# Performance work log

Measured on AMD Instinct MI355X. Metric: run time of the kernel, lower is better.

## Reference

```python
import jax, jax.numpy as jnp
import numpy as np

IN_DIMS = (8, 8, 8, 8)
OUT_DIMS = (8, 8, 8, 8)
RANK = 8
IN_FEATURES = 4096
OUT_FEATURES = 4096
BATCH = 4096


def setup_inputs() -> dict:
    key = jax.random.key(0)
    ks = jax.random.split(key, 6)
    scale = 1.0 / (IN_FEATURES ** 0.5)
    d = len(IN_DIMS)
    ranks = (1,) + (RANK,) * (d - 1) + (1,)
    cores = {}
    for k in range(d):
        shape = (ranks[k], IN_DIMS[k], OUT_DIMS[k], ranks[k + 1])
        # roughly balanced per-core scale so the dense-equivalent weight has ~1/sqrt(N) scale
        c_scale = scale ** (1.0 / d)
        cores[f"core_{k}"] = (jax.random.normal(ks[k + 1], shape, dtype=jnp.float32) * c_scale)
    x = jax.random.normal(ks[0], (BATCH, IN_FEATURES), dtype=jnp.float32)
    bias = jnp.zeros((OUT_FEATURES,), dtype=jnp.float32)
    return {"x": x, **cores, "bias": bias}


def _tt_contract(x, cores):
    # x: (B, N) with N = prod(IN_DIMS). Cores: core_k (r_{k-1}, i_k, o_k, r_k).
    # y[b, o1..od] = sum_{i,r} prod_k core_k[r_{k-1}, i_k, o_k, r_k] * x[b, i1..id]
    B = x.shape[0]
    d = len(IN_DIMS)
    # z: (Bo, r, i_k, suffix) where Bo = B * prod(out dims already contracted)
    z = x.reshape(B, 1, IN_DIMS[0], -1)
    for k, core in enumerate(cores):
        # contract current input mode and left rank against the core
        z = jnp.einsum("bris,riok->boks", z, core)  # (Bo, o_k, r_k, suffix)
        if k + 1 < d:
            Bo, ok, rk, s = z.shape
            z = z.reshape(Bo * ok, rk, IN_DIMS[k + 1], s // IN_DIMS[k + 1])
    return z.reshape(B, -1)  # (B, prod(OUT_DIMS))


def reference(x, core_0, core_1, core_2, core_3, bias):
    in_dtype = x.dtype
    xc = x.astype(core_0.dtype)
    y = _tt_contract(xc, (core_0, core_1, core_2, core_3))
    y = y + bias
    return y.astype(in_dtype)
```

## Files before the change

kernel.cpp:

```cpp
#include <hip/hip_runtime.h>
#include <hip/hip_bf16.h>


typedef __attribute__((ext_vector_type(8))) short bf16x8;
typedef __attribute__((ext_vector_type(4))) float f32x4;

#define MFMA16(a, b, c) __builtin_amdgcn_mfma_f32_16x16x32_bf16(a, b, c, 0, 0, 0)

__device__ __forceinline__ short f2bf(float f) {
    union { float f; unsigned u; } v{f};
    unsigned r = v.u + 0x7fff + ((v.u >> 16) & 1);
    return (short)(r >> 16);
}

__global__ void tt_prep(const float* __restrict__ c0, const float* __restrict__ c1,
                        const float* __restrict__ c2, const float* __restrict__ c3,
                        short* __restrict__ wpack) {
    int e    = blockIdx.x * 256 + threadIdx.x;
    int isV  = e >> 15;
    int idx  = e & 32767;
    int r2   = idx >> 12;
    int rem  = idx & 4095;
    int frag = rem >> 9;
    int lane = (rem >> 3) & 63;
    int j    = rem & 7;
    int nt = frag >> 1, kt = frag & 1;
    int k = kt * 32 + (lane >> 4) * 8 + j;
    int n = nt * 16 + (lane & 15);
    float acc = 0.f;
    if (!isV) {
        int i0 = k >> 3, i1 = k & 7, o0 = n >> 3, o1 = n & 7;
        #pragma unroll
        for (int r1 = 0; r1 < 8; ++r1)
            acc += c0[(i0 * 8 + o0) * 8 + r1] * c1[((r1 * 8 + i1) * 8 + o1) * 8 + r2];
    } else {
        int i2 = k >> 3, i3 = k & 7, o2 = n >> 3, o3 = n & 7;
        #pragma unroll
        for (int r3 = 0; r3 < 8; ++r3)
            acc += c2[((r2 * 8 + i2) * 8 + o2) * 8 + r3] * c3[(r3 * 8 + i3) * 8 + o3];
    }
    wpack[e] = f2bf(acc);
}

__global__ __launch_bounds__(512, 2)
void tt_main(const float* __restrict__ x, const float* __restrict__ bias,
             const short* __restrict__ wpack, float* __restrict__ out) {
    __shared__ short tbuf[8 * 4096];
    const int tid  = threadIdx.x;
    const int wave = tid >> 6;
    const int lane = tid & 63;
    const int lo   = lane & 15;
    const int q    = lane >> 4;
    const int b    = blockIdx.x * 8 + wave;

    short* T = &tbuf[wave * 4096];

    bf16x8 xa[4][2];
    const float* xb = x + (size_t)b * 4096;
    #pragma unroll
    for (int mt = 0; mt < 4; ++mt)
        #pragma unroll
        for (int kt = 0; kt < 2; ++kt)
            #pragma unroll
            for (int j = 0; j < 8; ++j) {
                int i01 = kt * 32 + q * 8 + j;
                int i23 = mt * 16 + lo;
                xa[mt][kt][j] = f2bf(xb[i01 * 64 + i23]);
            }

    f32x4 yacc[4][4];
    #pragma unroll
    for (int m = 0; m < 4; ++m)
        #pragma unroll
        for (int n = 0; n < 4; ++n)
            yacc[m][n] = f32x4{0.f, 0.f, 0.f, 0.f};

    const bf16x8* Up = (const bf16x8*)wpack;
    const bf16x8* Vp = (const bf16x8*)(wpack + 32768);

    for (int r2 = 0; r2 < 8; ++r2) {
        bf16x8 uf[4][2];
        #pragma unroll
        for (int nt = 0; nt < 4; ++nt)
            #pragma unroll
            for (int kt = 0; kt < 2; ++kt)
                uf[nt][kt] = Up[(r2 * 8 + nt * 2 + kt) * 64 + lane];

        #pragma unroll
        for (int mt = 0; mt < 4; ++mt) {
            f32x4 tacc[4];
            #pragma unroll
            for (int nt = 0; nt < 4; ++nt) tacc[nt] = f32x4{0.f, 0.f, 0.f, 0.f};
            #pragma unroll
            for (int kt = 0; kt < 2; ++kt)
                #pragma unroll
                for (int nt = 0; nt < 4; ++nt)
                    tacc[nt] = MFMA16(xa[mt][kt], uf[nt][kt], tacc[nt]);
            #pragma unroll
            for (int nt = 0; nt < 4; ++nt) {
                int o01 = nt * 16 + lo;
                int i23 = mt * 16 + q * 4;
                unsigned w0 = (unsigned)(unsigned short)f2bf(tacc[nt][0]) |
                              ((unsigned)(unsigned short)f2bf(tacc[nt][1]) << 16);
                unsigned w1 = (unsigned)(unsigned short)f2bf(tacc[nt][2]) |
                              ((unsigned)(unsigned short)f2bf(tacc[nt][3]) << 16);
                int byteoff = (o01 * 128 + i23 * 2) ^ ((o01 & 7) << 4);
                *(uint2*)((char*)T + byteoff) = make_uint2(w0, w1);
            }
        }

        bf16x8 vf[4][2];
        #pragma unroll
        for (int nt = 0; nt < 4; ++nt)
            #pragma unroll
            for (int kt = 0; kt < 2; ++kt)
                vf[nt][kt] = Vp[(r2 * 8 + nt * 2 + kt) * 64 + lane];

        #pragma unroll
        for (int kt = 0; kt < 2; ++kt) {
            bf16x8 ta[4];
            #pragma unroll
            for (int mt = 0; mt < 4; ++mt) {
                int o01 = mt * 16 + lo;
                int i23 = kt * 32 + q * 8;
                int byteoff = (o01 * 128 + i23 * 2) ^ ((o01 & 7) << 4);
                ta[mt] = *(const bf16x8*)((const char*)T + byteoff);
            }
            #pragma unroll
            for (int mt = 0; mt < 4; ++mt)
                #pragma unroll
                for (int nt = 0; nt < 4; ++nt)
                    yacc[mt][nt] = MFMA16(ta[mt], vf[nt][kt], yacc[mt][nt]);
        }
    }

    float* ob = out + (size_t)b * 4096;
    #pragma unroll
    for (int mt = 0; mt < 4; ++mt)
        #pragma unroll
        for (int nt = 0; nt < 4; ++nt)
            #pragma unroll
            for (int r = 0; r < 4; ++r) {
                int o01 = mt * 16 + q * 4 + r;
                int o23 = nt * 16 + lo;
                int no  = o01 * 64 + o23;
                ob[no] = yacc[mt][nt][r] + bias[no];
            }
}

extern "C" void kernel_launch(void* const* d_in, const int* in_sizes, int n_in,
                              void* d_out, int out_size, void* d_ws, size_t ws_size,
                              hipStream_t stream) {
    const float* x    = (const float*)d_in[0];
    const float* c0   = (const float*)d_in[1];
    const float* c1   = (const float*)d_in[2];
    const float* c2   = (const float*)d_in[3];
    const float* c3   = (const float*)d_in[4];
    const float* bias = (const float*)d_in[5];
    short* wpack = (short*)d_ws;

    tt_prep<<<256, 256, 0, stream>>>(c0, c1, c2, c3, wpack);
    tt_main<<<512, 512, 0, stream>>>(x, bias, wpack, (float*)d_out);
}
```

Measured before the change: 150.8 us.

## Switch to 32x32 MFMA and pass intermediate through registers via permlane swap

Reorders the two-stage contraction so the i23 modes are contracted first with 32x32x16 bf16 MFMA, and the intermediate is repacked in registers using permlane32_swap instead of being staged through LDS. The x load becomes vectorized float4 reads, and blocks shrink to 4 waves with twice as many blocks. This removes the LDS round trip and its synchronization-free but bandwidth-bound shared traffic, at the cost of more register pressure from 32x32 accumulators.

Measured after the change: 145.7 us. 1.04x faster.

```diff
diff --git a/kernel.cpp b/kernel.cpp
--- a/kernel.cpp
+++ b/kernel.cpp
@@ -3,148 +3,151 @@
 
 
 typedef __attribute__((ext_vector_type(8))) short bf16x8;
-typedef __attribute__((ext_vector_type(4))) float f32x4;
+typedef __attribute__((ext_vector_type(16))) float f32x16;
 
-#define MFMA16(a, b, c) __builtin_amdgcn_mfma_f32_16x16x32_bf16(a, b, c, 0, 0, 0)
+#define MFMA32(a, b, c) __builtin_amdgcn_mfma_f32_32x32x16_bf16(a, b, c, 0, 0, 0)
 
-__device__ __forceinline__ short f2bf(float f) {
-    union { float f; unsigned u; } v{f};
-    unsigned r = v.u + 0x7fff + ((v.u >> 16) & 1);
-    return (short)(r >> 16);
+__device__ __forceinline__ unsigned short bfu(float f) {
+    __hip_bfloat16 h = __float2bfloat16(f);
+    return *reinterpret_cast<unsigned short*>(&h);
+}
+__device__ __forceinline__ unsigned pk2(float a, float b) {
+    return (unsigned)bfu(a) | ((unsigned)bfu(b) << 16);
 }
 
 __global__ void tt_prep(const float* __restrict__ c0, const float* __restrict__ c1,
                         const float* __restrict__ c2, const float* __restrict__ c3,
-                        short* __restrict__ wpack) {
+                        unsigned short* __restrict__ wpack) {
     int e    = blockIdx.x * 256 + threadIdx.x;
-    int isV  = e >> 15;
-    int idx  = e & 32767;
-    int r2   = idx >> 12;
-    int rem  = idx & 4095;
-    int frag = rem >> 9;
-    int lane = (rem >> 3) & 63;
-    int j    = rem & 7;
-    int nt = frag >> 1, kt = frag & 1;
-    int k = kt * 32 + (lane >> 4) * 8 + j;
-    int n = nt * 16 + (lane & 15);
+    int lane = (e >> 3) & 63;
+    int j    = e & 7;
+    int hi   = lane >> 5, l31 = lane & 31;
     float acc = 0.f;
-    if (!isV) {
-        int i0 = k >> 3, i1 = k & 7, o0 = n >> 3, o1 = n & 7;
+    if (e < 32768) {
+        int idx = e;
+        int r2  = idx >> 12;
+        int nt  = (idx >> 11) & 1;
+        int ks1 = (idx >> 9) & 3;
+        int i23 = ks1 * 16 + hi * 8 + j;
+        int o23 = nt * 32 + l31;
+        int i2 = i23 >> 3, i3 = i23 & 7, o2 = o23 >> 3, o3 = o23 & 7;
+        #pragma unroll
+        for (int r3 = 0; r3 < 8; ++r3)
+            acc += c2[((r2 * 8 + i2) * 8 + o2) * 8 + r3] * c3[(r3 * 8 + i3) * 8 + o3];
+    } else {
+        int idx = e - 32768;
+        int r2  = idx >> 12;
+        int mt2 = (idx >> 11) & 1;
+        int kt  = (idx >> 10) & 1;
+        int ks2 = (idx >> 9) & 1;
+        int i01 = kt * 32 + ks2 * 16 + hi * 8 + j;
+        int o01 = mt2 * 32 + l31;
+        int i0 = i01 >> 3, i1 = i01 & 7, o0 = o01 >> 3, o1 = o01 & 7;
         #pragma unroll
         for (int r1 = 0; r1 < 8; ++r1)
             acc += c0[(i0 * 8 + o0) * 8 + r1] * c1[((r1 * 8 + i1) * 8 + o1) * 8 + r2];
-    } else {
-        int i2 = k >> 3, i3 = k & 7, o2 = n >> 3, o3 = n & 7;
-        #pragma unroll
-        for (int r3 = 0; r3 < 8; ++r3)
-            acc += c2[((r2 * 8 + i2) * 8 + o2) * 8 + r3] * c3[(r3 * 8 + i3) * 8 + o3];
     }
-    wpack[e] = f2bf(acc);
+    wpack[e] = bfu(acc);
 }
 
-__global__ __launch_bounds__(512, 2)
+__global__ __launch_bounds__(256, 2)
 void tt_main(const float* __restrict__ x, const float* __restrict__ bias,
-             const short* __restrict__ wpack, float* __restrict__ out) {
-    __shared__ short tbuf[8 * 4096];
-    const int tid  = threadIdx.x;
-    const int wave = tid >> 6;
-    const int lane = tid & 63;
-    const int lo   = lane & 15;
-    const int q    = lane >> 4;
-    const int b    = blockIdx.x * 8 + wave;
+             const unsigned short* __restrict__ wpack, float* __restrict__ out) {
+    const int lane = threadIdx.x & 63;
+    const int wave = threadIdx.x >> 6;
+    const int b    = blockIdx.x * 4 + wave;
+    const int l31  = lane & 31;
+    const int hi   = lane >> 5;
 
-    short* T = &tbuf[wave * 4096];
+    const float* xb = x + (size_t)b * 4096;
 
-    bf16x8 xa[4][2];
-    const float* xb = x + (size_t)b * 4096;
+    bf16x8 xa[2][4];
     #pragma unroll
-    for (int mt = 0; mt < 4; ++mt)
+    for (int mt = 0; mt < 2; ++mt)
         #pragma unroll
-        for (int kt = 0; kt < 2; ++kt)
-            #pragma unroll
-            for (int j = 0; j < 8; ++j) {
-                int i01 = kt * 32 + q * 8 + j;
-                int i23 = mt * 16 + lo;
-                xa[mt][kt][j] = f2bf(xb[i01 * 64 + i23]);
-            }
+        for (int ks1 = 0; ks1 < 4; ++ks1) {
+            const float* p = xb + (mt * 32 + l31) * 64 + ks1 * 16 + hi * 8;
+            float4 u0 = *(const float4*)p;
+            float4 u1 = *(const float4*)(p + 4);
+            union { unsigned w[4]; bf16x8 v; } t;
+            t.w[0] = pk2(u0.x, u0.y);
+            t.w[1] = pk2(u0.z, u0.w);
+            t.w[2] = pk2(u1.x, u1.y);
+            t.w[3] = pk2(u1.z, u1.w);
+            xa[mt][ks1] = t.v;
+        }
 
-    f32x4 yacc[4][4];
+    f32x16 yacc[2][2];
     #pragma unroll
-    for (int m = 0; m < 4; ++m)
+    for (int i = 0; i < 2; ++i)
         #pragma unroll
-        for (int n = 0; n < 4; ++n)
-            yacc[m][n] = f32x4{0.f, 0.f, 0.f, 0.f};
+        for (int k = 0; k < 2; ++k)
+            yacc[i][k] = (f32x16)0.0f;
 
-    const bf16x8* Up = (const bf16x8*)wpack;
-    const bf16x8* Vp = (const bf16x8*)(wpack + 32768);
+    const bf16x8* Vp = (const bf16x8*)wpack;
+    const bf16x8* Up = (const bf16x8*)(wpack + 32768);
 
     for (int r2 = 0; r2 < 8; ++r2) {
-        bf16x8 uf[4][2];
+        bf16x8 vf[2][4];
         #pragma unroll
-        for (int nt = 0; nt < 4; ++nt)
+        for (int nt = 0; nt < 2; ++nt)
             #pragma unroll
-            for (int kt = 0; kt < 2; ++kt)
-                uf[nt][kt] = Up[(r2 * 8 + nt * 2 + kt) * 64 + lane];
+            for (int ks1 = 0; ks1 < 4; ++ks1)
+                vf[nt][ks1] = Vp[((r2 * 2 + nt) * 4 + ks1) * 64 + lane];
 
         #pragma unroll
-        for (int mt = 0; mt < 4; ++mt) {
-            f32x4 tacc[4];
+        for (int mt = 0; mt < 2; ++mt) {
+            bf16x8 uf[2][2];
             #pragma unroll
-            for (int nt = 0; nt < 4; ++nt) tacc[nt] = f32x4{0.f, 0.f, 0.f, 0.f};
+            for (int mt2 = 0; mt2 < 2; ++mt2)
+                #pragma unroll
+                for (int ks2 = 0; ks2 < 2; ++ks2)
+                    uf[mt2][ks2] = Up[(((r2 * 2 + mt2) * 2 + mt) * 2 + ks2) * 64 + lane];
+
             #pragma unroll
-            for (int kt = 0; kt < 2; ++kt)
+            for (int nt = 0; nt < 2; ++nt) {
+                f32x16 s = (f32x16)0.0f;
                 #pragma unroll
-                for (int nt = 0; nt < 4; ++nt)
-                    tacc[nt] = MFMA16(xa[mt][kt], uf[nt][kt], tacc[nt]);
-            #pragma unroll
-            for (int nt = 0; nt < 4; ++nt) {
-                int o01 = nt * 16 + lo;
-                int i23 = mt * 16 + q * 4;
-                unsigned w0 = (unsigned)(unsigned short)f2bf(tacc[nt][0]) |
-                              ((unsigned)(unsigned short)f2bf(tacc[nt][1]) << 16);
-                unsigned w1 = (unsigned)(unsigned short)f2bf(tacc[nt][2]) |
-                              ((unsigned)(unsigned short)f2bf(tacc[nt][3]) << 16);
-                int byteoff = (o01 * 128 + i23 * 2) ^ ((o01 & 7) << 4);
-                *(uint2*)((char*)T + byteoff) = make_uint2(w0, w1);
+                for (int ks1 = 0; ks1 < 4; ++ks1)
+                    s = MFMA32(xa[mt][ks1], vf[nt][ks1], s);
+
+                bf16x8 bf[2];
+                #pragma unroll
+                for (int ks2 = 0; ks2 < 2; ++ks2) {
+                    unsigned A0 = pk2(s[8 * ks2 + 0], s[8 * ks2 + 1]);
+                    unsigned B0 = pk2(s[8 * ks2 + 2], s[8 * ks2 + 3]);
+                    unsigned A1 = pk2(s[8 * ks2 + 4], s[8 * ks2 + 5]);
+                    unsigned B1 = pk2(s[8 * ks2 + 6], s[8 * ks2 + 7]);
+                    auto rA = __builtin_amdgcn_permlane32_swap((int)A0, (int)A1, false, false);
+                    auto rB = __builtin_amdgcn_permlane32_swap((int)B0, (int)B1, false, false);
+                    union { unsigned w[4]; bf16x8 v; } t;
+                    t.w[0] = (unsigned)rA[0];
+                    t.w[1] = (unsigned)rB[0];
+                    t.w[2] = (unsigned)rA[1];
+                    t.w[3] = (unsigned)rB[1];
+                    bf[ks2] = t.v;
+                }
+
+                #pragma unroll
+                for (int mt2 = 0; mt2 < 2; ++mt2)
+                    #pragma unroll
+                    for (int ks2 = 0; ks2 < 2; ++ks2)
+                        yacc[mt2][nt] = MFMA32(uf[mt2][ks2], bf[ks2], yacc[mt2][nt]);
             }
-        }
-
-        bf16x8 vf[4][2];
-        #pragma unroll
-        for (int nt = 0; nt < 4; ++nt)
-            #pragma unroll
-            for (int kt = 0; kt < 2; ++kt)
-                vf[nt][kt] = Vp[(r2 * 8 + nt * 2 + kt) * 64 + lane];
-
-        #pragma unroll
-        for (int kt = 0; kt < 2; ++kt) {
-            bf16x8 ta[4];
-            #pragma unroll
-            for (int mt = 0; mt < 4; ++mt) {
-                int o01 = mt * 16 + lo;
-                int i23 = kt * 32 + q * 8;
-                int byteoff = (o01 * 128 + i23 * 2) ^ ((o01 & 7) << 4);
-                ta[mt] = *(const bf16x8*)((const char*)T + byteoff);
-            }
-            #pragma unroll
-            for (int mt = 0; mt < 4; ++mt)
-                #pragma unroll
-                for (int nt = 0; nt < 4; ++nt)
-                    yacc[mt][nt] = MFMA16(ta[mt], vf[nt][kt], yacc[mt][nt]);
         }
     }
 
     float* ob = out + (size_t)b * 4096;
     #pragma unroll
-    for (int mt = 0; mt < 4; ++mt)
+    for (int mt2 = 0; mt2 < 2; ++mt2)
         #pragma unroll
-        for (int nt = 0; nt < 4; ++nt)
+        for (int nt = 0; nt < 2; ++nt)
             #pragma unroll
-            for (int r = 0; r < 4; ++r) {
-                int o01 = mt * 16 + q * 4 + r;
-                int o23 = nt * 16 + lo;
-                int no  = o01 * 64 + o23;
-                ob[no] = yacc[mt][nt][r] + bias[no];
+            for (int r = 0; r < 16; ++r) {
+                int o01 = mt2 * 32 + (r & 3) + 8 * (r >> 2) + 4 * hi;
+                int o23 = nt * 32 + l31;
+                int off = o01 * 64 + o23;
+                ob[off] = yacc[mt2][nt][r] + bias[off];
             }
 }
 
@@ -157,8 +160,8 @@
     const float* c2   = (const float*)d_in[3];
     const float* c3   = (const float*)d_in[4];
     const float* bias = (const float*)d_in[5];
-    short* wpack = (short*)d_ws;
+    unsigned short* wpack = (unsigned short*)d_ws;
 
     tt_prep<<<256, 256, 0, stream>>>(c0, c1, c2, c3, wpack);
-    tt_main<<<512, 512, 0, stream>>>(x, bias, wpack, (float*)d_out);
+    tt_main<<<1024, 256, 0, stream>>>(x, bias, wpack, (float*)d_out);
 }
```
